# Performance work log

Hardware: AMD Instinct MI355X
Metric: run time of the kernel (lower is better)

The kernel has to match this reference:

```python
import jax, jax.numpy as jnp
from jax import lax
import numpy as np

N_TOOLS = 50
DIM = 512
N_TOKENS = 8192
PARAM_DIM = 256


def setup_inputs() -> dict:
    key = jax.random.key(0)
    ks = jax.random.split(key, 8)
    s = 1.0 / np.sqrt(DIM)
    x = jax.random.normal(ks[0], (N_TOKENS, DIM), dtype=jnp.float32)
    router_w = jax.random.uniform(ks[1], (N_TOOLS, DIM), jnp.float32, -s, s)
    router_b = jax.random.uniform(ks[2], (N_TOOLS,), jnp.float32, -s, s)
    expert_w = jax.random.uniform(ks[3], (N_TOOLS, DIM, DIM), jnp.float32, -s, s)
    expert_b = jax.random.uniform(ks[4], (N_TOOLS, DIM), jnp.float32, -s, s)
    param_w = jax.random.uniform(ks[5], (PARAM_DIM, DIM), jnp.float32, -s, s)
    param_b = jax.random.uniform(ks[6], (PARAM_DIM,), jnp.float32, -s, s)
    return {"x": x, "router_w": router_w, "router_b": router_b,
            "expert_w": expert_w, "expert_b": expert_b,
            "param_w": param_w, "param_b": param_b}


def _moe_adapt(x, tool_idx, expert_w, expert_b):
    # Top-1 dispatch: for each expert i, y_i = x @ W_i.T + b_i, written only
    # where tool_idx == i. Scan over the fixed 50 experts (mirrors the torch
    # masked per-expert Linear loop) with masked select instead of scatter.
    def step(acc, wb):
        i, W, b = wb
        y = x @ W.T + b  # [N, dim]
        mask = (tool_idx == i)[:, None]
        return jnp.where(mask, y, acc), None

    init = jnp.zeros_like(x)
    acc, _ = lax.scan(step, init, (jnp.arange(N_TOOLS), expert_w, expert_b))
    return acc


def reference(x, router_w, router_b, expert_w, expert_b, param_w, param_b):
    tool_logits = x @ router_w.T + router_b            # [N, 50]
    tool_probs = jax.nn.softmax(tool_logits, axis=-1)   # [N, 50]
    tool_idx = jnp.argmax(tool_probs, axis=-1)          # [N] int
    adapted = _moe_adapt(x, tool_idx, expert_w, expert_b)  # [N, dim]
    params = x @ param_w.T + param_b                    # [N, 256]
    return (tool_idx, tool_probs, adapted, params)
```

## Files before the change

### kernel.cpp

```cpp
#include <hip/hip_runtime.h>
#include <hip/hip_bf16.h>
#include <math.h>

#define N_TOKENS 8192
#define DIM      512
#define N_TOOLS  50
#define PARAM_DIM 256
#define N_ROWBLK (N_TOKENS / 64)
#define MAX_BATCHES 192
#define LDSS 72

typedef float  f32x4 __attribute__((ext_vector_type(4)));
typedef short  s16x8 __attribute__((ext_vector_type(8)));
typedef short  s16x4 __attribute__((ext_vector_type(4)));

#define WS_IDX     0
#define WS_HIST    8192
#define WS_PHIST   14592
#define WS_OFFSETS 20992
#define WS_COUNTS  21056
#define WS_ORDER   21120
#define WS_BE      29312
#define WS_BM0     29504
#define WS_NB      29696
#define WS_XH      32768
#define WS_XL      2130944

__device__ inline float bf2f(short s) {
    return __uint_as_float(((unsigned)(unsigned short)s) << 16);
}

__device__ inline s16x4 pk4(float a, float b, float c, float d) {
    __hip_bfloat162 p0 = __float22bfloat162_rn(make_float2(a, b));
    __hip_bfloat162 p1 = __float22bfloat162_rn(make_float2(c, d));
    union { __hip_bfloat162 h; short2 s; } u0, u1;
    u0.h = p0; u1.h = p1;
    s16x4 r; r[0] = u0.s.x; r[1] = u0.s.y; r[2] = u1.s.x; r[3] = u1.s.y;
    return r;
}

__global__ __launch_bounds__(256) void cvt_x_kernel(const float* __restrict__ x,
                                                    short* __restrict__ xh,
                                                    short* __restrict__ xl) {
    size_t i = (size_t)(blockIdx.x * 256 + threadIdx.x) * 4;
    float4 v = *(const float4*)&x[i];
    s16x4 h = pk4(v.x, v.y, v.z, v.w);
    s16x4 l = pk4(v.x - bf2f(h[0]), v.y - bf2f(h[1]),
                  v.z - bf2f(h[2]), v.w - bf2f(h[3]));
    *(s16x4*)&xh[i] = h;
    *(s16x4*)&xl[i] = l;
}

__global__ __launch_bounds__(256) void head_mfma(const short* __restrict__ xh,
                                                 const short* __restrict__ xl,
                                                 const float* __restrict__ pw,
                                                 const float* __restrict__ pb,
                                                 const float* __restrict__ rw,
                                                 const float* __restrict__ rb,
                                                 float* __restrict__ out_params,
                                                 float* __restrict__ probs,
                                                 float* __restrict__ out_idx,
                                                 int* __restrict__ idx_i,
                                                 int* __restrict__ hist) {
    int r0 = blockIdx.y * 64;
    bool isl = (blockIdx.x == 4);
    int c0 = isl ? 0 : blockIdx.x * 64;

    __shared__ short As[64 * LDSS];
    __shared__ short Bs[64 * LDSS];
    __shared__ short Al[64 * LDSS];
    __shared__ short Bl[64 * LDSS];
    __shared__ int rowcol[64];

    int tid = threadIdx.x;
    int wv = tid >> 6;
    int lane = tid & 63;
    int fm = lane & 15;
    int q = lane >> 4;

    const float* Bsrc = isl ? rw : pw;

    int ar0 = tid >> 3, ag = tid & 7;
    int ar1 = ar0 + 32;
    const short* aptr0 = xh + (size_t)(r0 + ar0) * DIM + ag * 8;
    const short* aptr1 = xh + (size_t)(r0 + ar1) * DIM + ag * 8;
    const short* alptr0 = xl + (size_t)(r0 + ar0) * DIM + ag * 8;
    const short* alptr1 = xl + (size_t)(r0 + ar1) * DIM + ag * 8;
    int bc[4], bg[4];
    const float* bptr[4];
#pragma unroll
    for (int i = 0; i < 4; ++i) {
        int u = i * 256 + tid;
        bc[i] = u >> 4; bg[i] = u & 15;
        bptr[i] = Bsrc + (size_t)(c0 + bc[i]) * DIM + bg[i] * 4;
    }

    f32x4 acc[4] = {{0.f, 0.f, 0.f, 0.f}, {0.f, 0.f, 0.f, 0.f},
                    {0.f, 0.f, 0.f, 0.f}, {0.f, 0.f, 0.f, 0.f}};

    s16x8 apre0, apre1, alpre0, alpre1;
    float4 bpre[4];
    apre0 = *(const s16x8*)aptr0;
    apre1 = *(const s16x8*)aptr1;
    if (isl) { alpre0 = *(const s16x8*)alptr0; alpre1 = *(const s16x8*)alptr1; }
#pragma unroll
    for (int i = 0; i < 4; ++i) {
        float4 v = {0.f, 0.f, 0.f, 0.f};
        if (!isl || bc[i] < N_TOOLS) v = *(const float4*)bptr[i];
        bpre[i] = v;
    }

    for (int k0 = 0; k0 < DIM; k0 += 64) {
        *(s16x8*)&As[ar0 * LDSS + ag * 8] = apre0;
        *(s16x8*)&As[ar1 * LDSS + ag * 8] = apre1;
        if (isl) {
            *(s16x8*)&Al[ar0 * LDSS + ag * 8] = alpre0;
            *(s16x8*)&Al[ar1 * LDSS + ag * 8] = alpre1;
        }
#pragma unroll
        for (int i = 0; i < 4; ++i) {
            float4 v = bpre[i];
            s16x4 h = pk4(v.x, v.y, v.z, v.w);
            *(s16x4*)&Bs[bc[i] * LDSS + bg[i] * 4] = h;
            if (isl) {
                s16x4 l = pk4(v.x - bf2f(h[0]), v.y - bf2f(h[1]),
                              v.z - bf2f(h[2]), v.w - bf2f(h[3]));
                *(s16x4*)&Bl[bc[i] * LDSS + bg[i] * 4] = l;
            }
        }
        __syncthreads();

        int kn = k0 + 64;
        if (kn < DIM) {
            apre0 = *(const s16x8*)(aptr0 + kn);
            apre1 = *(const s16x8*)(aptr1 + kn);
            if (isl) {
                alpre0 = *(const s16x8*)(alptr0 + kn);
                alpre1 = *(const s16x8*)(alptr1 + kn);
            }
#pragma unroll
            for (int i = 0; i < 4; ++i) {
                float4 v = {0.f, 0.f, 0.f, 0.f};
                if (!isl || bc[i] < N_TOOLS) v = *(const float4*)(bptr[i] + kn);
                bpre[i] = v;
            }
        }

#pragma unroll
        for (int kk = 0; kk < 64; kk += 32) {
            int ao = (wv * 16 + fm) * LDSS + kk + q * 8;
            s16x8 a = *(const s16x8*)&As[ao];
            if (!isl) {
#pragma unroll
                for (int n = 0; n < 4; ++n) {
                    s16x8 b = *(const s16x8*)&Bs[(n * 16 + fm) * LDSS + kk + q * 8];
                    acc[n] = __builtin_amdgcn_mfma_f32_16x16x32_bf16(a, b, acc[n], 0, 0, 0);
                }
            } else {
                s16x8 al = *(const s16x8*)&Al[ao];
#pragma unroll
                for (int n = 0; n < 4; ++n) {
                    int bo = (n * 16 + fm) * LDSS + kk + q * 8;
                    s16x8 b  = *(const s16x8*)&Bs[bo];
                    s16x8 bl = *(const s16x8*)&Bl[bo];
                    acc[n] = __builtin_amdgcn_mfma_f32_16x16x32_bf16(a,  b,  acc[n], 0, 0, 0);
                    acc[n] = __builtin_amdgcn_mfma_f32_16x16x32_bf16(a,  bl, acc[n], 0, 0, 0);
                    acc[n] = __builtin_amdgcn_mfma_f32_16x16x32_bf16(al, b,  acc[n], 0, 0, 0);
                }
            }
        }
        __syncthreads();
    }

    if (!isl) {
        float bias[4];
#pragma unroll
        for (int n = 0; n < 4; ++n) bias[n] = pb[c0 + n * 16 + fm];
#pragma unroll
        for (int r = 0; r < 4; ++r) {
            int row = r0 + wv * 16 + q * 4 + r;
            float* op = out_params + (size_t)row * PARAM_DIM + c0;
#pragma unroll
            for (int n = 0; n < 4; ++n) op[n * 16 + fm] = acc[n][r] + bias[n];
        }
    } else {
        float rbv[4];
#pragma unroll
        for (int n = 0; n < 4; ++n) {
            int c = n * 16 + fm;
            rbv[n] = (c < N_TOOLS) ? rb[c] : 0.f;
        }
#pragma unroll
        for (int rr = 0; rr < 4; ++rr) {
            int row_l = wv * 16 + q * 4 + rr;
            int row = r0 + row_l;
            float v[4];
            float vmax = -INFINITY; int vcol = N_TOOLS;
#pragma unroll
            for (int n = 0; n < 4; ++n) {
                int c = n * 16 + fm;
                v[n] = acc[n][rr] + rbv[n];
                if (c < N_TOOLS && v[n] > vmax) { vmax = v[n]; vcol = c; }
            }
#pragma unroll
            for (int s = 1; s < 16; s <<= 1) {
                float om = __shfl_xor(vmax, s, 64);
                int   oc = __shfl_xor(vcol, s, 64);
                if (om > vmax || (om == vmax && oc < vcol)) { vmax = om; vcol = oc; }
            }
            float e[4]; float esum = 0.f;
#pragma unroll
            for (int n = 0; n < 4; ++n) {
                int c = n * 16 + fm;
                e[n] = (c < N_TOOLS) ? expf(v[n] - vmax) : 0.f;
                esum += e[n];
            }
#pragma unroll
            for (int s = 1; s < 16; s <<= 1) esum += __shfl_xor(esum, s, 64);
            float inv = 1.f / esum;
#pragma unroll
            for (int n = 0; n < 4; ++n) {
                int c = n * 16 + fm;
                if (c < N_TOOLS) probs[(size_t)row * N_TOOLS + c] = e[n] * inv;
            }
            if (fm == 0) {
                out_idx[row] = (float)vcol;
                idx_i[row] = vcol;
                rowcol[row_l] = vcol;
            }
        }
        __syncthreads();
        if (wv == 0) {
            int myc = rowcol[lane];
            int cnt = 0;
            for (int e2 = 0; e2 < N_TOOLS; ++e2) {
                unsigned long long m = __ballot(myc == e2);
                if (lane == e2) cnt = __popcll(m);
            }
            if (lane < N_TOOLS) hist[blockIdx.y * N_TOOLS + lane] = cnt;
        }
    }
}

__global__ void scan1_kernel(const int* __restrict__ hist,
                             int* __restrict__ phist,
                             int* __restrict__ counts) {
    int e = blockIdx.x;
    int l = threadIdx.x;
    int v0 = hist[l * N_TOOLS + e];
    int v1 = hist[(64 + l) * N_TOOLS + e];
    int s0 = v0;
#pragma unroll
    for (int s = 1; s < 64; s <<= 1) {
        int t = __shfl_up(s0, s, 64);
        if (l >= s) s0 += t;
    }
    int tot0 = __shfl(s0, 63, 64);
    int s1 = v1;
#pragma unroll
    for (int s = 1; s < 64; s <<= 1) {
        int t = __shfl_up(s1, s, 64);
        if (l >= s) s1 += t;
    }
    s1 += tot0;
    phist[l * N_TOOLS + e] = s0 - v0;
    phist[(64 + l) * N_TOOLS + e] = s1 - v1;
    if (l == 63) counts[e] = s1;
}

__global__ void scan2_kernel(const int* __restrict__ counts,
                             int* __restrict__ offsets,
                             int* __restrict__ batch_e,
                             int* __restrict__ batch_m0,
                             int* __restrict__ nb_out) {
    int lane = threadIdx.x;
    int c = (lane < N_TOOLS) ? counts[lane] : 0;
    int pre = c;
#pragma unroll
    for (int s = 1; s < 64; s <<= 1) {
        int v = __shfl_up(pre, s, 64);
        if (lane >= s) pre += v;
    }
    if (lane < N_TOOLS) offsets[lane] = pre - c;

    int nb_i = (lane < N_TOOLS) ? (c + 63) >> 6 : 0;
    int pre2 = nb_i;
#pragma unroll
    for (int s = 1; s < 64; s <<= 1) {
        int v = __shfl_up(pre2, s, 64);
        if (lane >= s) pre2 += v;
    }
    int bstart = pre2 - nb_i;
    for (int b = 0; b < nb_i; ++b) {
        batch_e[bstart + b] = lane;
        batch_m0[bstart + b] = b * 64;
    }
    if (lane == 63) nb_out[0] = pre2;
}

__global__ void reorder_kernel(const int* __restrict__ idx_i,
                               const int* __restrict__ offsets,
                               const int* __restrict__ phist,
                               int* __restrict__ order) {
    int b = blockIdx.x;
    int lane = threadIdx.x;
    int t = b * 64 + lane;
    int e = idx_i[t];
    unsigned long long lt = (1ull << lane) - 1ull;
    int rank = 0;
    for (int ex = 0; ex < N_TOOLS; ++ex) {
        unsigned long long m = __ballot(e == ex);
        if (e == ex) rank = __popcll(m & lt);
    }
    order[offsets[e] + phist[b * N_TOOLS + e] + rank] = t;
}

__global__ __launch_bounds__(256) void adapted_mfma(const short* __restrict__ xh,
                                                    const float* __restrict__ ew,
                                                    const float* __restrict__ eb,
                                                    const int* __restrict__ order,
                                                    const int* __restrict__ batch_e,
                                                    const int* __restrict__ batch_m0,
                                                    const int* __restrict__ nb_ptr,
                                                    const int* __restrict__ offsets,
                                                    const int* __restrict__ counts,
                                                    float* __restrict__ out) {
    int b = blockIdx.y;
    if (b >= nb_ptr[0]) return;
    int e = batch_e[b];
    int m0 = batch_m0[b];
    int c0 = blockIdx.x * 64;
    int start = offsets[e] + m0;
    int len = counts[e] - m0;
    if (len > 64) len = 64;

    __shared__ short As[64 * LDSS];
    __shared__ short Bs[64 * LDSS];
    __shared__ int toks[64];

    int tid = threadIdx.x;
    if (tid < 64) toks[tid] = (tid < len) ? order[start + tid] : -1;
    __syncthreads();

    int wv = tid >> 6;
    int lane = tid & 63;
    int fm = lane & 15;
    int q = lane >> 4;

    const float* We = ew + (size_t)e * DIM * DIM;

    int ar0 = tid >> 3, ag = tid & 7;
    int ar1 = ar0 + 32;
    int tok0 = toks[ar0], tok1 = toks[ar1];
    const short* aptr0 = (tok0 >= 0) ? xh + (size_t)tok0 * DIM + ag * 8 : nullptr;
    const short* aptr1 = (tok1 >= 0) ? xh + (size_t)tok1 * DIM + ag * 8 : nullptr;
    int bc[4], bg[4];
    const float* bptr[4];
#pragma unroll
    for (int i = 0; i < 4; ++i) {
        int u = i * 256 + tid;
        bc[i] = u >> 4; bg[i] = u & 15;
        bptr[i] = We + (size_t)(c0 + bc[i]) * DIM + bg[i] * 4;
    }

    f32x4 acc[4] = {{0.f, 0.f, 0.f, 0.f}, {0.f, 0.f, 0.f, 0.f},
                    {0.f, 0.f, 0.f, 0.f}, {0.f, 0.f, 0.f, 0.f}};

    const s16x8 z8 = {0, 0, 0, 0, 0, 0, 0, 0};
    s16x8 apre0 = aptr0 ? *(const s16x8*)aptr0 : z8;
    s16x8 apre1 = aptr1 ? *(const s16x8*)aptr1 : z8;
    float4 bpre[4];
#pragma unroll
    for (int i = 0; i < 4; ++i) bpre[i] = *(const float4*)bptr[i];

    for (int k0 = 0; k0 < DIM; k0 += 64) {
        *(s16x8*)&As[ar0 * LDSS + ag * 8] = apre0;
        *(s16x8*)&As[ar1 * LDSS + ag * 8] = apre1;
#pragma unroll
        for (int i = 0; i < 4; ++i) {
            float4 v = bpre[i];
            *(s16x4*)&Bs[bc[i] * LDSS + bg[i] * 4] = pk4(v.x, v.y, v.z, v.w);
        }
        __syncthreads();

        int kn = k0 + 64;
        if (kn < DIM) {
            apre0 = aptr0 ? *(const s16x8*)(aptr0 + kn) : z8;
            apre1 = aptr1 ? *(const s16x8*)(aptr1 + kn) : z8;
#pragma unroll
            for (int i = 0; i < 4; ++i) bpre[i] = *(const float4*)(bptr[i] + kn);
        }

#pragma unroll
        for (int kk = 0; kk < 64; kk += 32) {
            s16x8 a = *(const s16x8*)&As[(wv * 16 + fm) * LDSS + kk + q * 8];
#pragma unroll
            for (int n = 0; n < 4; ++n) {
                s16x8 bf = *(const s16x8*)&Bs[(n * 16 + fm) * LDSS + kk + q * 8];
                acc[n] = __builtin_amdgcn_mfma_f32_16x16x32_bf16(a, bf, acc[n], 0, 0, 0);
            }
        }
        __syncthreads();
    }

    float bias[4];
#pragma unroll
    for (int n = 0; n < 4; ++n) bias[n] = eb[(size_t)e * DIM + c0 + n * 16 + fm];

#pragma unroll
    for (int r = 0; r < 4; ++r) {
        int row = wv * 16 + q * 4 + r;
        int tok = toks[row];
        if (tok < 0) continue;
        float* op = out + (size_t)tok * DIM + c0;
#pragma unroll
        for (int n = 0; n < 4; ++n) op[n * 16 + fm] = acc[n][r] + bias[n];
    }
}

extern "C" void kernel_launch(void* const* d_in, const int* in_sizes, int n_in,
                              void* d_out, int out_size, void* d_ws, size_t ws_size,
                              hipStream_t stream) {
    const float* x        = (const float*)d_in[0];
    const float* router_w = (const float*)d_in[1];
    const float* router_b = (const float*)d_in[2];
    const float* expert_w = (const float*)d_in[3];
    const float* expert_b = (const float*)d_in[4];
    const float* param_w  = (const float*)d_in[5];
    const float* param_b  = (const float*)d_in[6];

    float* out = (float*)d_out;
    float* out_idx     = out;
    float* out_probs   = out + N_TOKENS;
    float* out_adapted = out + N_TOKENS + N_TOKENS * N_TOOLS;
    float* out_params  = out_adapted + (size_t)N_TOKENS * DIM;

    int* ws = (int*)d_ws;
    int* ws_idx     = ws + WS_IDX;
    int* ws_hist    = ws + WS_HIST;
    int* ws_phist   = ws + WS_PHIST;
    int* ws_offsets = ws + WS_OFFSETS;
    int* ws_counts  = ws + WS_COUNTS;
    int* ws_order   = ws + WS_ORDER;
    int* ws_be      = ws + WS_BE;
    int* ws_bm0     = ws + WS_BM0;
    int* ws_nb      = ws + WS_NB;
    short* ws_xh    = (short*)(ws + WS_XH);
    short* ws_xl    = (short*)(ws + WS_XL);

    cvt_x_kernel<<<N_TOKENS * DIM / 4 / 256, 256, 0, stream>>>(x, ws_xh, ws_xl);

    head_mfma<<<dim3(5, N_ROWBLK), 256, 0, stream>>>(ws_xh, ws_xl, param_w, param_b,
                                                     router_w, router_b,
                                                     out_params, out_probs,
                                                     out_idx, ws_idx, ws_hist);

    scan1_kernel<<<N_TOOLS, 64, 0, stream>>>(ws_hist, ws_phist, ws_counts);

    scan2_kernel<<<1, 64, 0, stream>>>(ws_counts, ws_offsets, ws_be, ws_bm0, ws_nb);

    reorder_kernel<<<N_ROWBLK, 64, 0, stream>>>(ws_idx, ws_offsets, ws_phist, ws_order);

    adapted_mfma<<<dim3(8, MAX_BATCHES), 256, 0, stream>>>(ws_xh, expert_w, expert_b,
                                                           ws_order, ws_be, ws_bm0, ws_nb,
                                                           ws_offsets, ws_counts, out_adapted);
}
```

Measured before the change: 155.8 us.

## Enlarge expert GEMM tiles to 128x128, split params GEMM out, fuse scans

The expert GEMM now processes batches of 128 tokens by 128 output columns per block, with 2x8 MFMA accumulators per wave. Fewer batches per expert means each expert's fp32 weights are re-read fewer times, at the cost of more padding waste for partial batches. The params projection moves from the head kernel into its own 128x128-tiled kernel, leaving a logits-only kernel. The two scan kernels are merged into one 1024-thread launch that uses 128-row batching. These changes add register pressure and LDS use per block, and produce fewer blocks for the expert GEMM.

Measured after the change: 166.4 us. 6.8% more time.

```diff
diff --git a/kernel.cpp b/kernel.cpp
--- a/kernel.cpp
+++ b/kernel.cpp
@@ -7,7 +7,7 @@
 #define N_TOOLS  50
 #define PARAM_DIM 256
 #define N_ROWBLK (N_TOKENS / 64)
-#define MAX_BATCHES 192
+#define MAX_BATCHES 128
 #define LDSS 72
 
 typedef float  f32x4 __attribute__((ext_vector_type(4)));
@@ -51,24 +51,19 @@
     *(s16x4*)&xl[i] = l;
 }
 
-__global__ __launch_bounds__(256) void head_mfma(const short* __restrict__ xh,
-                                                 const short* __restrict__ xl,
-                                                 const float* __restrict__ pw,
-                                                 const float* __restrict__ pb,
-                                                 const float* __restrict__ rw,
-                                                 const float* __restrict__ rb,
-                                                 float* __restrict__ out_params,
-                                                 float* __restrict__ probs,
-                                                 float* __restrict__ out_idx,
-                                                 int* __restrict__ idx_i,
-                                                 int* __restrict__ hist) {
-    int r0 = blockIdx.y * 64;
-    bool isl = (blockIdx.x == 4);
-    int c0 = isl ? 0 : blockIdx.x * 64;
+__global__ __launch_bounds__(256) void logits_mfma(const short* __restrict__ xh,
+                                                   const short* __restrict__ xl,
+                                                   const float* __restrict__ rw,
+                                                   const float* __restrict__ rb,
+                                                   float* __restrict__ probs,
+                                                   float* __restrict__ out_idx,
+                                                   int* __restrict__ idx_i,
+                                                   int* __restrict__ hist) {
+    int r0 = blockIdx.x * 64;
 
     __shared__ short As[64 * LDSS];
+    __shared__ short Al[64 * LDSS];
     __shared__ short Bs[64 * LDSS];
-    __shared__ short Al[64 * LDSS];
     __shared__ short Bl[64 * LDSS];
     __shared__ int rowcol[64];
 
@@ -78,12 +73,10 @@
     int fm = lane & 15;
     int q = lane >> 4;
 
-    const float* Bsrc = isl ? rw : pw;
-
     int ar0 = tid >> 3, ag = tid & 7;
     int ar1 = ar0 + 32;
-    const short* aptr0 = xh + (size_t)(r0 + ar0) * DIM + ag * 8;
-    const short* aptr1 = xh + (size_t)(r0 + ar1) * DIM + ag * 8;
+    const short* aptr0  = xh + (size_t)(r0 + ar0) * DIM + ag * 8;
+    const short* aptr1  = xh + (size_t)(r0 + ar1) * DIM + ag * 8;
     const short* alptr0 = xl + (size_t)(r0 + ar0) * DIM + ag * 8;
     const short* alptr1 = xl + (size_t)(r0 + ar1) * DIM + ag * 8;
     int bc[4], bg[4];
@@ -92,41 +85,37 @@
     for (int i = 0; i < 4; ++i) {
         int u = i * 256 + tid;
         bc[i] = u >> 4; bg[i] = u & 15;
-        bptr[i] = Bsrc + (size_t)(c0 + bc[i]) * DIM + bg[i] * 4;
+        bptr[i] = rw + (size_t)bc[i] * DIM + bg[i] * 4;
     }
 
     f32x4 acc[4] = {{0.f, 0.f, 0.f, 0.f}, {0.f, 0.f, 0.f, 0.f},
                     {0.f, 0.f, 0.f, 0.f}, {0.f, 0.f, 0.f, 0.f}};
 
-    s16x8 apre0, apre1, alpre0, alpre1;
+    s16x8 apre0 = *(const s16x8*)aptr0;
+    s16x8 apre1 = *(const s16x8*)aptr1;
+    s16x8 alpre0 = *(const s16x8*)alptr0;
+    s16x8 alpre1 = *(const s16x8*)alptr1;
     float4 bpre[4];
-    apre0 = *(const s16x8*)aptr0;
-    apre1 = *(const s16x8*)aptr1;
-    if (isl) { alpre0 = *(const s16x8*)alptr0; alpre1 = *(const s16x8*)alptr1; }
 #pragma unroll
     for (int i = 0; i < 4; ++i) {
         float4 v = {0.f, 0.f, 0.f, 0.f};
-        if (!isl || bc[i] < N_TOOLS) v = *(const float4*)bptr[i];
+        if (bc[i] < N_TOOLS) v = *(const float4*)bptr[i];
         bpre[i] = v;
     }
 
     for (int k0 = 0; k0 < DIM; k0 += 64) {
         *(s16x8*)&As[ar0 * LDSS + ag * 8] = apre0;
         *(s16x8*)&As[ar1 * LDSS + ag * 8] = apre1;
-        if (isl) {
-            *(s16x8*)&Al[ar0 * LDSS + ag * 8] = alpre0;
-            *(s16x8*)&Al[ar1 * LDSS + ag * 8] = alpre1;
-        }
+        *(s16x8*)&Al[ar0 * LDSS + ag * 8] = alpre0;
+        *(s16x8*)&Al[ar1 * LDSS + ag * 8] = alpre1;
 #pragma unroll
         for (int i = 0; i < 4; ++i) {
             float4 v = bpre[i];
             s16x4 h = pk4(v.x, v.y, v.z, v.w);
             *(s16x4*)&Bs[bc[i] * LDSS + bg[i] * 4] = h;
-            if (isl) {
-                s16x4 l = pk4(v.x - bf2f(h[0]), v.y - bf2f(h[1]),
-                              v.z - bf2f(h[2]), v.w - bf2f(h[3]));
-                *(s16x4*)&Bl[bc[i] * LDSS + bg[i] * 4] = l;
-            }
+            s16x4 l = pk4(v.x - bf2f(h[0]), v.y - bf2f(h[1]),
+                          v.z - bf2f(h[2]), v.w - bf2f(h[3]));
+            *(s16x4*)&Bl[bc[i] * LDSS + bg[i] * 4] = l;
         }
         __syncthreads();
 
@@ -134,14 +123,12 @@
         if (kn < DIM) {
             apre0 = *(const s16x8*)(aptr0 + kn);
             apre1 = *(const s16x8*)(aptr1 + kn);
-            if (isl) {
-                alpre0 = *(const s16x8*)(alptr0 + kn);
-                alpre1 = *(const s16x8*)(alptr1 + kn);
-            }
+            alpre0 = *(const s16x8*)(alptr0 + kn);
+            alpre1 = *(const s16x8*)(alptr1 + kn);
 #pragma unroll
             for (int i = 0; i < 4; ++i) {
                 float4 v = {0.f, 0.f, 0.f, 0.f};
-                if (!isl || bc[i] < N_TOOLS) v = *(const float4*)(bptr[i] + kn);
+                if (bc[i] < N_TOOLS) v = *(const float4*)(bptr[i] + kn);
                 bpre[i] = v;
             }
         }
@@ -149,153 +136,227 @@
 #pragma unroll
         for (int kk = 0; kk < 64; kk += 32) {
             int ao = (wv * 16 + fm) * LDSS + kk + q * 8;
-            s16x8 a = *(const s16x8*)&As[ao];
-            if (!isl) {
-#pragma unroll
-                for (int n = 0; n < 4; ++n) {
-                    s16x8 b = *(const s16x8*)&Bs[(n * 16 + fm) * LDSS + kk + q * 8];
-                    acc[n] = __builtin_amdgcn_mfma_f32_16x16x32_bf16(a, b, acc[n], 0, 0, 0);
-                }
-            } else {
-                s16x8 al = *(const s16x8*)&Al[ao];
-#pragma unroll
-                for (int n = 0; n < 4; ++n) {
-                    int bo = (n * 16 + fm) * LDSS + kk + q * 8;
-                    s16x8 b  = *(const s16x8*)&Bs[bo];
-                    s16x8 bl = *(const s16x8*)&Bl[bo];
-                    acc[n] = __builtin_amdgcn_mfma_f32_16x16x32_bf16(a,  b,  acc[n], 0, 0, 0);
-                    acc[n] = __builtin_amdgcn_mfma_f32_16x16x32_bf16(a,  bl, acc[n], 0, 0, 0);
-                    acc[n] = __builtin_amdgcn_mfma_f32_16x16x32_bf16(al, b,  acc[n], 0, 0, 0);
-                }
+            s16x8 a  = *(const s16x8*)&As[ao];
+            s16x8 al = *(const s16x8*)&Al[ao];
+#pragma unroll
+            for (int n = 0; n < 4; ++n) {
+                int bo = (n * 16 + fm) * LDSS + kk + q * 8;
+                s16x8 b  = *(const s16x8*)&Bs[bo];
+                s16x8 bl = *(const s16x8*)&Bl[bo];
+                acc[n] = __builtin_amdgcn_mfma_f32_16x16x32_bf16(a,  b,  acc[n], 0, 0, 0);
+                acc[n] = __builtin_amdgcn_mfma_f32_16x16x32_bf16(a,  bl, acc[n], 0, 0, 0);
+                acc[n] = __builtin_amdgcn_mfma_f32_16x16x32_bf16(al, b,  acc[n], 0, 0, 0);
             }
         }
         __syncthreads();
     }
 
-    if (!isl) {
-        float bias[4];
-#pragma unroll
-        for (int n = 0; n < 4; ++n) bias[n] = pb[c0 + n * 16 + fm];
-#pragma unroll
-        for (int r = 0; r < 4; ++r) {
-            int row = r0 + wv * 16 + q * 4 + r;
-            float* op = out_params + (size_t)row * PARAM_DIM + c0;
-#pragma unroll
-            for (int n = 0; n < 4; ++n) op[n * 16 + fm] = acc[n][r] + bias[n];
-        }
-    } else {
-        float rbv[4];
+    float rbv[4];
+#pragma unroll
+    for (int n = 0; n < 4; ++n) {
+        int c = n * 16 + fm;
+        rbv[n] = (c < N_TOOLS) ? rb[c] : 0.f;
+    }
+#pragma unroll
+    for (int rr = 0; rr < 4; ++rr) {
+        int row_l = wv * 16 + q * 4 + rr;
+        int row = r0 + row_l;
+        float v[4];
+        float vmax = -INFINITY; int vcol = N_TOOLS;
 #pragma unroll
         for (int n = 0; n < 4; ++n) {
             int c = n * 16 + fm;
-            rbv[n] = (c < N_TOOLS) ? rb[c] : 0.f;
-        }
-#pragma unroll
-        for (int rr = 0; rr < 4; ++rr) {
-            int row_l = wv * 16 + q * 4 + rr;
-            int row = r0 + row_l;
-            float v[4];
-            float vmax = -INFINITY; int vcol = N_TOOLS;
-#pragma unroll
-            for (int n = 0; n < 4; ++n) {
-                int c = n * 16 + fm;
-                v[n] = acc[n][rr] + rbv[n];
-                if (c < N_TOOLS && v[n] > vmax) { vmax = v[n]; vcol = c; }
+            v[n] = acc[n][rr] + rbv[n];
+            if (c < N_TOOLS && v[n] > vmax) { vmax = v[n]; vcol = c; }
+        }
+#pragma unroll
+        for (int s = 1; s < 16; s <<= 1) {
+            float om = __shfl_xor(vmax, s, 64);
+            int   oc = __shfl_xor(vcol, s, 64);
+            if (om > vmax || (om == vmax && oc < vcol)) { vmax = om; vcol = oc; }
+        }
+        float e[4]; float esum = 0.f;
+#pragma unroll
+        for (int n = 0; n < 4; ++n) {
+            int c = n * 16 + fm;
+            e[n] = (c < N_TOOLS) ? expf(v[n] - vmax) : 0.f;
+            esum += e[n];
+        }
+#pragma unroll
+        for (int s = 1; s < 16; s <<= 1) esum += __shfl_xor(esum, s, 64);
+        float inv = 1.f / esum;
+#pragma unroll
+        for (int n = 0; n < 4; ++n) {
+            int c = n * 16 + fm;
+            if (c < N_TOOLS) probs[(size_t)row * N_TOOLS + c] = e[n] * inv;
+        }
+        if (fm == 0) {
+            out_idx[row] = (float)vcol;
+            idx_i[row] = vcol;
+            rowcol[row_l] = vcol;
+        }
+    }
+    __syncthreads();
+    if (wv == 0) {
+        int myc = rowcol[lane];
+        int cnt = 0;
+        for (int e2 = 0; e2 < N_TOOLS; ++e2) {
+            unsigned long long m = __ballot(myc == e2);
+            if (lane == e2) cnt = __popcll(m);
+        }
+        if (lane < N_TOOLS) hist[blockIdx.x * N_TOOLS + lane] = cnt;
+    }
+}
+
+__global__ __launch_bounds__(256) void params_mfma(const short* __restrict__ xh,
+                                                   const float* __restrict__ pw,
+                                                   const float* __restrict__ pb,
+                                                   float* __restrict__ out) {
+    int r0 = blockIdx.y * 128;
+    int c0 = blockIdx.x * 128;
+
+    __shared__ short As[128 * LDSS];
+    __shared__ short Bs[128 * LDSS];
+
+    int tid = threadIdx.x;
+    int wv = tid >> 6;
+    int lane = tid & 63;
+    int fm = lane & 15;
+    int q = lane >> 4;
+
+    int arb = tid >> 3, ag = tid & 7;
+    const short* aptr[4];
+#pragma unroll
+    for (int i = 0; i < 4; ++i)
+        aptr[i] = xh + (size_t)(r0 + arb + 32 * i) * DIM + ag * 8;
+    int bcb = tid >> 4, bg = tid & 15;
+    const float* bptr[8];
+#pragma unroll
+    for (int i = 0; i < 8; ++i)
+        bptr[i] = pw + (size_t)(c0 + bcb + 16 * i) * DIM + bg * 4;
+
+    f32x4 acc[2][8];
+#pragma unroll
+    for (int m = 0; m < 2; ++m)
+#pragma unroll
+        for (int n = 0; n < 8; ++n) acc[m][n] = {0.f, 0.f, 0.f, 0.f};
+
+    s16x8 apre[4];
+    float4 bpre[8];
+#pragma unroll
+    for (int i = 0; i < 4; ++i) apre[i] = *(const s16x8*)aptr[i];
+#pragma unroll
+    for (int i = 0; i < 8; ++i) bpre[i] = *(const float4*)bptr[i];
+
+    for (int k0 = 0; k0 < DIM; k0 += 64) {
+#pragma unroll
+        for (int i = 0; i < 4; ++i)
+            *(s16x8*)&As[(arb + 32 * i) * LDSS + ag * 8] = apre[i];
+#pragma unroll
+        for (int i = 0; i < 8; ++i) {
+            float4 v = bpre[i];
+            *(s16x4*)&Bs[(bcb + 16 * i) * LDSS + bg * 4] = pk4(v.x, v.y, v.z, v.w);
+        }
+        __syncthreads();
+
+        int kn = k0 + 64;
+        if (kn < DIM) {
+#pragma unroll
+            for (int i = 0; i < 4; ++i) apre[i] = *(const s16x8*)(aptr[i] + kn);
+#pragma unroll
+            for (int i = 0; i < 8; ++i) bpre[i] = *(const float4*)(bptr[i] + kn);
+        }
+
+#pragma unroll
+        for (int kk = 0; kk < 64; kk += 32) {
+            s16x8 a[2];
+#pragma unroll
+            for (int m = 0; m < 2; ++m)
+                a[m] = *(const s16x8*)&As[(wv * 32 + m * 16 + fm) * LDSS + kk + q * 8];
+#pragma unroll
+            for (int n = 0; n < 8; ++n) {
+                s16x8 b = *(const s16x8*)&Bs[(n * 16 + fm) * LDSS + kk + q * 8];
+#pragma unroll
+                for (int m = 0; m < 2; ++m)
+                    acc[m][n] = __builtin_amdgcn_mfma_f32_16x16x32_bf16(a[m], b, acc[m][n], 0, 0, 0);
             }
-#pragma unroll
-            for (int s = 1; s < 16; s <<= 1) {
-                float om = __shfl_xor(vmax, s, 64);
-                int   oc = __shfl_xor(vcol, s, 64);
-                if (om > vmax || (om == vmax && oc < vcol)) { vmax = om; vcol = oc; }
-            }
-            float e[4]; float esum = 0.f;
-#pragma unroll
-            for (int n = 0; n < 4; ++n) {
-                int c = n * 16 + fm;
-                e[n] = (c < N_TOOLS) ? expf(v[n] - vmax) : 0.f;
-                esum += e[n];
-            }
-#pragma unroll
-            for (int s = 1; s < 16; s <<= 1) esum += __shfl_xor(esum, s, 64);
-            float inv = 1.f / esum;
-#pragma unroll
-            for (int n = 0; n < 4; ++n) {
-                int c = n * 16 + fm;
-                if (c < N_TOOLS) probs[(size_t)row * N_TOOLS + c] = e[n] * inv;
-            }
-            if (fm == 0) {
-                out_idx[row] = (float)vcol;
-                idx_i[row] = vcol;
-                rowcol[row_l] = vcol;
-            }
         }
         __syncthreads();
-        if (wv == 0) {
-            int myc = rowcol[lane];
-            int cnt = 0;
-            for (int e2 = 0; e2 < N_TOOLS; ++e2) {
-                unsigned long long m = __ballot(myc == e2);
-                if (lane == e2) cnt = __popcll(m);
-            }
-            if (lane < N_TOOLS) hist[blockIdx.y * N_TOOLS + lane] = cnt;
-        }
-    }
-}
-
-__global__ void scan1_kernel(const int* __restrict__ hist,
-                             int* __restrict__ phist,
-                             int* __restrict__ counts) {
-    int e = blockIdx.x;
-    int l = threadIdx.x;
-    int v0 = hist[l * N_TOOLS + e];
-    int v1 = hist[(64 + l) * N_TOOLS + e];
-    int s0 = v0;
-#pragma unroll
-    for (int s = 1; s < 64; s <<= 1) {
-        int t = __shfl_up(s0, s, 64);
-        if (l >= s) s0 += t;
-    }
-    int tot0 = __shfl(s0, 63, 64);
-    int s1 = v1;
-#pragma unroll
-    for (int s = 1; s < 64; s <<= 1) {
-        int t = __shfl_up(s1, s, 64);
-        if (l >= s) s1 += t;
-    }
-    s1 += tot0;
-    phist[l * N_TOOLS + e] = s0 - v0;
-    phist[(64 + l) * N_TOOLS + e] = s1 - v1;
-    if (l == 63) counts[e] = s1;
-}
-
-__global__ void scan2_kernel(const int* __restrict__ counts,
-                             int* __restrict__ offsets,
-                             int* __restrict__ batch_e,
-                             int* __restrict__ batch_m0,
-                             int* __restrict__ nb_out) {
-    int lane = threadIdx.x;
-    int c = (lane < N_TOOLS) ? counts[lane] : 0;
-    int pre = c;
-#pragma unroll
-    for (int s = 1; s < 64; s <<= 1) {
-        int v = __shfl_up(pre, s, 64);
-        if (lane >= s) pre += v;
-    }
-    if (lane < N_TOOLS) offsets[lane] = pre - c;
-
-    int nb_i = (lane < N_TOOLS) ? (c + 63) >> 6 : 0;
-    int pre2 = nb_i;
-#pragma unroll
-    for (int s = 1; s < 64; s <<= 1) {
-        int v = __shfl_up(pre2, s, 64);
-        if (lane >= s) pre2 += v;
-    }
-    int bstart = pre2 - nb_i;
-    for (int b = 0; b < nb_i; ++b) {
-        batch_e[bstart + b] = lane;
-        batch_m0[bstart + b] = b * 64;
-    }
-    if (lane == 63) nb_out[0] = pre2;
+    }
+
+    float bias[8];
+#pragma unroll
+    for (int n = 0; n < 8; ++n) bias[n] = pb[c0 + n * 16 + fm];
+
+#pragma unroll
+    for (int m = 0; m < 2; ++m)
+#pragma unroll
+        for (int r = 0; r < 4; ++r) {
+            int row = r0 + wv * 32 + m * 16 + q * 4 + r;
+            float* op = out + (size_t)row * PARAM_DIM + c0;
+#pragma unroll
+            for (int n = 0; n < 8; ++n) op[n * 16 + fm] = acc[m][n][r] + bias[n];
+        }
+}
+
+__global__ __launch_bounds__(1024) void scan_all(const int* __restrict__ hist,
+                                                 int* __restrict__ phist,
+                                                 int* __restrict__ counts,
+                                                 int* __restrict__ offsets,
+                                                 int* __restrict__ batch_e,
+                                                 int* __restrict__ batch_m0,
+                                                 int* __restrict__ nb_out) {
+    __shared__ int cnt_s[64];
+    int l = threadIdx.x & 63;
+    int w = threadIdx.x >> 6;
+
+    for (int e = w; e < N_TOOLS; e += 16) {
+        int v0 = hist[l * N_TOOLS + e];
+        int v1 = hist[(64 + l) * N_TOOLS + e];
+        int s0 = v0;
+#pragma unroll
+        for (int s = 1; s < 64; s <<= 1) {
+            int t = __shfl_up(s0, s, 64);
+            if (l >= s) s0 += t;
+        }
+        int tot0 = __shfl(s0, 63, 64);
+        int s1 = v1;
+#pragma unroll
+        for (int s = 1; s < 64; s <<= 1) {
+            int t = __shfl_up(s1, s, 64);
+            if (l >= s) s1 += t;
+        }
+        s1 += tot0;
+        phist[l * N_TOOLS + e] = s0 - v0;
+        phist[(64 + l) * N_TOOLS + e] = s1 - v1;
+        if (l == 63) cnt_s[e] = s1;
+    }
+    __syncthreads();
+
+    if (w == 0) {
+        int c = (l < N_TOOLS) ? cnt_s[l] : 0;
+        int pre = c;
+#pragma unroll
+        for (int s = 1; s < 64; s <<= 1) {
+            int v = __shfl_up(pre, s, 64);
+            if (l >= s) pre += v;
+        }
+        if (l < N_TOOLS) { offsets[l] = pre - c; counts[l] = c; }
+
+        int nb_i = (l < N_TOOLS) ? (c + 127) >> 7 : 0;
+        int pre2 = nb_i;
+#pragma unroll
+        for (int s = 1; s < 64; s <<= 1) {
+            int v = __shfl_up(pre2, s, 64);
+            if (l >= s) pre2 += v;
+        }
+        int bstart = pre2 - nb_i;
+        for (int b = 0; b < nb_i; ++b) {
+            batch_e[bstart + b] = l;
+            batch_m0[bstart + b] = b * 128;
+        }
+        if (l == 63) nb_out[0] = pre2;
+    }
 }
 
 __global__ void reorder_kernel(const int* __restrict__ idx_i,
@@ -329,17 +390,17 @@
     if (b >= nb_ptr[0]) return;
     int e = batch_e[b];
     int m0 = batch_m0[b];
-    int c0 = blockIdx.x * 64;
+    int c0 = blockIdx.x * 128;
     int start = offsets[e] + m0;
     int len = counts[e] - m0;
-    if (len > 64) len = 64;
-
-    __shared__ short As[64 * LDSS];
-    __shared__ short Bs[64 * LDSS];
-    __shared__ int toks[64];
+    if (len > 128) len = 128;
+
+    __shared__ short As[128 * LDSS];
+    __shared__ short Bs[128 * LDSS];
+    __shared__ int toks[128];
 
     int tid = threadIdx.x;
-    if (tid < 64) toks[tid] = (tid < len) ? order[start + tid] : -1;
+    if (tid < 128) toks[tid] = (tid < len) ? order[start + tid] : -1;
     __syncthreads();
 
     int wv = tid >> 6;
@@ -349,73 +410,85 @@
 
     const float* We = ew + (size_t)e * DIM * DIM;
 
-    int ar0 = tid >> 3, ag = tid & 7;
-    int ar1 = ar0 + 32;
-    int tok0 = toks[ar0], tok1 = toks[ar1];
-    const short* aptr0 = (tok0 >= 0) ? xh + (size_t)tok0 * DIM + ag * 8 : nullptr;
-    const short* aptr1 = (tok1 >= 0) ? xh + (size_t)tok1 * DIM + ag * 8 : nullptr;
-    int bc[4], bg[4];
-    const float* bptr[4];
+    int arb = tid >> 3, ag = tid & 7;
+    const short* aptr[4];
 #pragma unroll
     for (int i = 0; i < 4; ++i) {
-        int u = i * 256 + tid;
-        bc[i] = u >> 4; bg[i] = u & 15;
-        bptr[i] = We + (size_t)(c0 + bc[i]) * DIM + bg[i] * 4;
-    }
-
-    f32x4 acc[4] = {{0.f, 0.f, 0.f, 0.f}, {0.f, 0.f, 0.f, 0.f},
-                    {0.f, 0.f, 0.f, 0.f}, {0.f, 0.f, 0.f, 0.f}};
+        int tok = toks[arb + 32 * i];
+        aptr[i] = (tok >= 0) ? xh + (size_t)tok * DIM + ag * 8 : nullptr;
+    }
+    int bcb = tid >> 4, bg = tid & 15;
+    const float* bptr[8];
+#pragma unroll
+    for (int i = 0; i < 8; ++i)
+        bptr[i] = We + (size_t)(c0 + bcb + 16 * i) * DIM + bg * 4;
+
+    f32x4 acc[2][8];
+#pragma unroll
+    for (int m = 0; m < 2; ++m)
+#pragma unroll
+        for (int n = 0; n < 8; ++n) acc[m][n] = {0.f, 0.f, 0.f, 0.f};
 
     const s16x8 z8 = {0, 0, 0, 0, 0, 0, 0, 0};
-    s16x8 apre0 = aptr0 ? *(const s16x8*)aptr0 : z8;
-    s16x8 apre1 = aptr1 ? *(const s16x8*)aptr1 : z8;
-    float4 bpre[4];
-#pragma unroll
-    for (int i = 0; i < 4; ++i) bpre[i] = *(const float4*)bptr[i];
+    s16x8 apre[4];
+    float4 bpre[8];
+#pragma unroll
+    for (int i = 0; i < 4; ++i) apre[i] = aptr[i] ? *(const s16x8*)aptr[i] : z8;
+#pragma unroll
+    for (int i = 0; i < 8; ++i) bpre[i] = *(const float4*)bptr[i];
 
     for (int k0 = 0; k0 < DIM; k0 += 64) {
-        *(s16x8*)&As[ar0 * LDSS + ag * 8] = apre0;
-        *(s16x8*)&As[ar1 * LDSS + ag * 8] = apre1;
-#pragma unroll
-        for (int i = 0; i < 4; ++i) {
+#pragma unroll
+        for (int i = 0; i < 4; ++i)
+            *(s16x8*)&As[(arb + 32 * i) * LDSS + ag * 8] = apre[i];
+#pragma unroll
+        for (int i = 0; i < 8; ++i) {
             float4 v = bpre[i];
-            *(s16x4*)&Bs[bc[i] * LDSS + bg[i] * 4] = pk4(v.x, v.y, v.z, v.w);
+            *(s16x4*)&Bs[(bcb + 16 * i) * LDSS + bg * 4] = pk4(v.x, v.y, v.z, v.w);
         }
         __syncthreads();
 
         int kn = k0 + 64;
         if (kn < DIM) {
-            apre0 = aptr0 ? *(const s16x8*)(aptr0 + kn) : z8;
-            apre1 = aptr1 ? *(const s16x8*)(aptr1 + kn) : z8;
-#pragma unroll
-            for (int i = 0; i < 4; ++i) bpre[i] = *(const float4*)(bptr[i] + kn);
+#pragma unroll
+            for (int i = 0; i < 4; ++i)
+                apre[i] = aptr[i] ? *(const s16x8*)(aptr[i] + kn) : z8;
+#pragma unroll
+            for (int i = 0; i < 8; ++i) bpre[i] = *(const float4*)(bptr[i] + kn);
         }
 
 #pragma unroll
         for (int kk = 0; kk < 64; kk += 32) {
-            s16x8 a = *(const s16x8*)&As[(wv * 16 + fm) * LDSS + kk + q * 8];
-#pragma unroll
-            for (int n = 0; n < 4; ++n) {
+            s16x8 a[2];
+#pragma unroll
+            for (int m = 0; m < 2; ++m)
+                a[m] = *(const s16x8*)&As[(wv * 32 + m * 16 + fm) * LDSS + kk + q * 8];
+#pragma unroll
+            for (int n = 0; n < 8; ++n) {
                 s16x8 bf = *(const s16x8*)&Bs[(n * 16 + fm) * LDSS + kk + q * 8];
-                acc[n] = __builtin_amdgcn_mfma_f32_16x16x32_bf16(a, bf, acc[n], 0, 0, 0);
+#pragma unroll
+                for (int m = 0; m < 2; ++m)
+                    acc[m][n] = __builtin_amdgcn_mfma_f32_16x16x32_bf16(a[m], bf, acc[m][n], 0, 0, 0);
             }
         }
         __syncthreads();
     }
 
-    float bias[4];
-#pragma unroll
-    for (int n = 0; n < 4; ++n) bias[n] = eb[(size_t)e * DIM + c0 + n * 16 + fm];
-
-#pragma unroll
-    for (int r = 0; r < 4; ++r) {
-        int row = wv * 16 + q * 4 + r;
-        int tok = toks[row];
-        if (tok < 0) continue;
-        float* op = out + (size_t)tok * DIM + c0;
-#pragma unroll
-        for (int n = 0; n < 4; ++n) op[n * 16 + fm] = acc[n][r] + bias[n];
-    }
+    float bias[8];
+#pragma unroll
+    for (int n = 0; n < 8; ++n) bias[n] = eb[(size_t)e * DIM + c0 + n * 16 + fm];
+
+#pragma unroll
+    for (int m = 0; m < 2; ++m)
+#pragma unroll
+        for (int r = 0; r < 4; ++r) {
+            int row = wv * 32 + m * 16 + q * 4 + r;
+            int tok = toks[row];
+            if (tok < 0) continue;
+            float* op = out + (size_t)tok * DIM + c0;
+#pragma unroll
+            for (int n = 0; n < 8; ++n) op[n * 16 + fm] = acc[m][n][r] + bias[n];
+        }
 }
 
 extern "C" void kernel_launch(void* const* d_in, const int* in_sizes, int n_in,
@@ -450,18 +523,17 @@
 
     cvt_x_kernel<<<N_TOKENS * DIM / 4 / 256, 256, 0, stream>>>(x, ws_xh, ws_xl);
 
-    head_mfma<<<dim3(5, N_ROWBLK), 256, 0, stream>>>(ws_xh, ws_xl, param_w, param_b,
-                                                     router_w, router_b,
-                                                     out_params, out_probs,
-                                                     out_idx, ws_idx, ws_hist);
-
-    scan1_kernel<<<N_TOOLS, 64, 0, stream>>>(ws_hist, ws_phist, ws_counts);
-
-    scan2_kernel<<<1, 64, 0, stream>>>(ws_counts, ws_offsets, ws_be, ws_bm0, ws_nb);
+    logits_mfma<<<N_ROWBLK, 256, 0, stream>>>(ws_xh, ws_xl, router_w, router_b,
+                                              out_probs, out_idx, ws_idx, ws_hist);
+
+    scan_all<<<1, 1024, 0, stream>>>(ws_hist, ws_phist, ws_counts, ws_offsets,
+                                     ws_be, ws_bm0, ws_nb);
 
     reorder_kernel<<<N_ROWBLK, 64, 0, stream>>>(ws_idx, ws_offsets, ws_phist, ws_order);
 
-    adapted_mfma<<<dim3(8, MAX_BATCHES), 256, 0, stream>>>(ws_xh, expert_w, expert_b,
+    params_mfma<<<dim3(2, 64), 256, 0, stream>>>(ws_xh, param_w, param_b, out_params);
+
+    adapted_mfma<<<dim3(4, MAX_BATCHES), 256, 0, stream>>>(ws_xh, expert_w, expert_b,
                                                            ws_order, ws_be, ws_bm0, ws_nb,
                                                            ws_offsets, ws_counts, out_adapted);
 }
```
